# Kernel optimization log

Measured on AMD Instinct MI355X. Metric: run time of the kernel, lower is better.

## Reference

```python
import jax, jax.numpy as jnp
import numpy as np

TOPK = 20
BN_EPS = 1e-5
NEG_SLOPE = 0.2  # DGL GAT default leaky_relu slope


def setup_inputs() -> dict:
    B, N, Ft, D = 128, 512, 64, 64
    key = jax.random.key(0)
    ks = jax.random.split(key, 6)
    return {
        "data": jax.random.normal(ks[0], (B, N, Ft), jnp.float32),
        "emb": jax.random.normal(ks[1], (N, D), jnp.float32) * 0.5,
        "fc_w": jax.random.normal(ks[2], (D, Ft), jnp.float32) * (1.0 / np.sqrt(Ft)),
        "fc_b": jnp.zeros((D,), jnp.float32),
        "attn_w": jax.random.normal(ks[3], (4 * D,), jnp.float32) * (1.0 / np.sqrt(4 * D)),
        "attn_b": jnp.zeros((), jnp.float32),
        "bn_gamma": jnp.ones((D,), jnp.float32),
        "bn_beta": jnp.zeros((D,), jnp.float32),
        "out_w": jax.random.normal(ks[4], (D,), jnp.float32) * (1.0 / np.sqrt(D)),
        "out_b": jnp.zeros((), jnp.float32),
    }


def reference(data, emb, fc_w, fc_b, attn_w, attn_b, bn_gamma, bn_beta, out_w, out_b):
    B, N, Ft = data.shape
    D = emb.shape[-1]

    # --- dynamic graph build from detached embeddings (cosine-sim topk) ---
    w = jax.lax.stop_gradient(emb)
    nrm = jnp.linalg.norm(w, axis=-1)
    cos = (w @ w.T) / (nrm[:, None] * nrm[None, :])      # [N, N]
    _, topk_idx = jax.lax.top_k(cos, TOPK)               # [N, TOPK]
    src = topk_idx.reshape(-1)                           # gated_j (message sources)
    dst = jnp.tile(jnp.arange(N), TOPK)                  # gated_i = arange(N).repeat(1,topk).flatten()

    # --- GAT layer: z = W x + b ; edge score from concat([z, emb]) at both ends ---
    z = jnp.einsum("bnf,df->bnd", data, fc_w) + fc_b     # [B, N, D]
    key_feat = jnp.concatenate([z, jnp.broadcast_to(emb, (B, N, D))], axis=-1)  # [B, N, 2D]
    a_src, a_dst = attn_w[: 2 * D], attn_w[2 * D :]
    s_src = jnp.einsum("bnd,d->bn", key_feat, a_src)
    s_dst = jnp.einsum("bnd,d->bn", key_feat, a_dst)
    e = jax.nn.leaky_relu(s_src[:, src] + s_dst[:, dst] + attn_b, NEG_SLOPE)    # [B, E]

    # segment softmax over incoming edges of each dst node (same edges every batch)
    m = jnp.full((B, N), -jnp.inf, e.dtype).at[:, dst].max(e)
    p = jnp.exp(e - m[:, dst])
    denom = jnp.zeros((B, N), e.dtype).at[:, dst].add(p)
    alpha = p / denom[:, dst]                            # [B, E]

    # scatter-aggregate messages
    h = jnp.zeros_like(z).at[:, dst].add(alpha[..., None] * z[:, src])          # [B, N, D]

    # --- trailing dense: mul by embedding, BatchNorm1d over channel D, relu, linear ---
    rst = h * emb[None]                                  # [B, N, D]
    mu = rst.mean(axis=(0, 1))
    var = rst.var(axis=(0, 1))
    rst = jax.nn.relu((rst - mu) / jnp.sqrt(var + BN_EPS) * bn_gamma + bn_beta)
    out = jnp.einsum("bnd,d->bn", rst, out_w) + out_b    # [B, N]
    return out
```

## Files before the change

### kernel.cpp

```cpp
#include <hip/hip_runtime.h>

#define NN 512
#define DD 64
#define TOPK 20
#define BB 128

__global__ __launch_bounds__(256) void k1_pre(const float* __restrict__ data,
                                              const float* __restrict__ emb,
                                              const float* __restrict__ fc_w,
                                              const float* __restrict__ fc_b,
                                              const float* __restrict__ attn_w,
                                              float* __restrict__ es_src,
                                              float* __restrict__ es_dst,
                                              double* __restrict__ gstats,
                                              float* __restrict__ z,
                                              float* __restrict__ zsrc,
                                              float* __restrict__ zdst,
                                              int* __restrict__ topk) {
    __shared__ __align__(16) char smem[34816];
    const int bid = blockIdx.x, t = threadIdx.x;

    if (bid < 512) {
        const int i = bid;
        double* cosrow = (double*)smem;
        double* nrmv   = (double*)(smem + 4096);
        float4* A4     = (float4*)(smem + 8192);
        const float4* e4 = (const float4*)emb;

        if (t < 16) A4[t] = e4[i * 16 + t];
        __syncthreads();

        #pragma unroll
        for (int jj = 0; jj < 2; ++jj) {
            const int j = jj * 256 + t;
            double dot = 0.0, ss = 0.0;
            #pragma unroll
            for (int c = 0; c < 16; ++c) {
                const float4 a = A4[c];
                const float4 b = e4[j * 16 + c];
                dot += (double)a.x * (double)b.x;
                dot += (double)a.y * (double)b.y;
                dot += (double)a.z * (double)b.z;
                dot += (double)a.w * (double)b.w;
                const double vx = b.x, vy = b.y, vz = b.z, vw = b.w;
                ss += vx * vx; ss += vy * vy; ss += vz * vz; ss += vw * vw;
            }
            cosrow[j] = dot;
            nrmv[j]   = sqrt(ss);
        }
        __syncthreads();

        if (t < 64) {
            const int lane = t;
            const double nrm_i = nrmv[i];
            double v[8];
            #pragma unroll
            for (int s = 0; s < 8; ++s)
                v[s] = cosrow[s * 64 + lane] / (nrm_i * nrmv[s * 64 + lane]);

            for (int k = 0; k < TOPK; ++k) {
                double bv = v[0]; int bs = 0;
                #pragma unroll
                for (int s = 1; s < 8; ++s) if (v[s] > bv) { bv = v[s]; bs = s; }
                int bi2 = bs * 64 + lane;
                #pragma unroll
                for (int off = 32; off > 0; off >>= 1) {
                    double ov = __shfl_xor(bv, off);
                    int    oi = __shfl_xor(bi2, off);
                    if (ov > bv || (ov == bv && oi < bi2)) { bv = ov; bi2 = oi; }
                }
                if (lane == 0) topk[i * TOPK + k] = bi2;
                if ((bi2 & 63) == lane) v[bi2 >> 6] = -1e300;
            }
        }
    } else if (bid < 1536) {
        float (*As)[68]  = (float(*)[68])smem;
        float (*WsT)[68] = (float(*)[68])(smem + 17408);
        const long r0 = (long)(bid - 512) * 64;
        const float4* data4 = (const float4*)data;
        const float4* fcw4  = (const float4*)fc_w;

        for (int m = t; m < 1024; m += 256) {
            const int r = m >> 4, c4 = m & 15;
            *(float4*)&As[r][c4 * 4] = data4[(r0 + r) * 16 + c4];
        }
        for (int m = t; m < 1024; m += 256) {
            const int d = m >> 4, f4 = m & 15;
            float4 v = fcw4[d * 16 + f4];
            WsT[f4 * 4 + 0][d] = v.x;
            WsT[f4 * 4 + 1][d] = v.y;
            WsT[f4 * 4 + 2][d] = v.z;
            WsT[f4 * 4 + 3][d] = v.w;
        }
        __syncthreads();

        const int tr = t >> 4, tc = t & 15;
        float acc[4][4] = {};
        for (int k0 = 0; k0 < 64; k0 += 4) {
            float4 a4[4], b4[4];
            #pragma unroll
            for (int i = 0; i < 4; ++i) a4[i] = *(float4*)&As[tr * 4 + i][k0];
            #pragma unroll
            for (int kk = 0; kk < 4; ++kk) b4[kk] = *(float4*)&WsT[k0 + kk][tc * 4];
            #pragma unroll
            for (int i = 0; i < 4; ++i) {
                acc[i][0] += a4[i].x * b4[0].x + a4[i].y * b4[1].x + a4[i].z * b4[2].x + a4[i].w * b4[3].x;
                acc[i][1] += a4[i].x * b4[0].y + a4[i].y * b4[1].y + a4[i].z * b4[2].y + a4[i].w * b4[3].y;
                acc[i][2] += a4[i].x * b4[0].z + a4[i].y * b4[1].z + a4[i].z * b4[2].z + a4[i].w * b4[3].z;
                acc[i][3] += a4[i].x * b4[0].w + a4[i].y * b4[1].w + a4[i].z * b4[2].w + a4[i].w * b4[3].w;
            }
        }
        float bias[4], aw0[4], aw2[4];
        #pragma unroll
        for (int j = 0; j < 4; ++j) {
            bias[j] = fc_b[tc * 4 + j];
            aw0[j]  = attn_w[tc * 4 + j];
            aw2[j]  = attn_w[128 + tc * 4 + j];
        }
        float zb[4][4];
        #pragma unroll
        for (int i = 0; i < 4; ++i) {
            #pragma unroll
            for (int j = 0; j < 4; ++j) zb[i][j] = acc[i][j] + bias[j];
            float4 vv; vv.x = zb[i][0]; vv.y = zb[i][1]; vv.z = zb[i][2]; vv.w = zb[i][3];
            *(float4*)&z[(r0 + tr * 4 + i) * 64 + tc * 4] = vv;
        }
        __syncthreads();

        float (*redA)[17] = (float(*)[17])smem;
        float (*redB)[17] = (float(*)[17])(smem + 4352);
        #pragma unroll
        for (int i = 0; i < 4; ++i) {
            redA[tr * 4 + i][tc] = zb[i][0] * aw0[0] + zb[i][1] * aw0[1] + zb[i][2] * aw0[2] + zb[i][3] * aw0[3];
            redB[tr * 4 + i][tc] = zb[i][0] * aw2[0] + zb[i][1] * aw2[1] + zb[i][2] * aw2[2] + zb[i][3] * aw2[3];
        }
        __syncthreads();
        if (t < 64) {
            float sA = 0.f, sB = 0.f;
            #pragma unroll
            for (int k = 0; k < 16; ++k) { sA += redA[t][k]; sB += redB[t][k]; }
            zsrc[r0 + t] = sA;
            zdst[r0 + t] = sB;
        }
    } else {
        #pragma unroll
        for (int jj = 0; jj < 2; ++jj) {
            const int j = jj * 256 + t;
            float s1 = 0.f, s2 = 0.f;
            #pragma unroll
            for (int c = 0; c < 64; ++c) {
                const float w = emb[j * 64 + c];
                s1 += w * attn_w[64 + c];
                s2 += w * attn_w[192 + c];
            }
            es_src[j] = s1;
            es_dst[j] = s2;
        }
        if (t < 128) gstats[t] = 0.0;
    }
}

__global__ __launch_bounds__(256) void k3_attn(const float* __restrict__ z,
                                               const float* __restrict__ zsrc,
                                               const float* __restrict__ zdst,
                                               const float* __restrict__ es_src,
                                               const float* __restrict__ es_dst,
                                               const int* __restrict__ topk,
                                               const float* __restrict__ emb,
                                               const float* __restrict__ attn_b_p,
                                               float* __restrict__ rst,
                                               double* __restrict__ gstats) {
    __shared__ float  zs[512 * 16];
    __shared__ double alf_pool[2560];
    __shared__ unsigned short sIdx[256 * 20];
    float* alf = (float*)alf_pool;
    const float4* alf4 = (const float4*)alf_pool;

    const int b    = blockIdx.x >> 2;
    const int dq   = blockIdx.x & 3;
    const int doff = dq * 16;
    const int t    = threadIdx.x;
    const float attn_b = *attn_b_p;
    const long b512 = (long)b * NN;

    float4* zs4 = (float4*)zs;
    for (int m = t; m < 2048; m += 256) {
        const int n = m >> 2, c4i = m & 3;
        zs4[m] = *(const float4*)(z + (b512 + n) * 64 + doff + c4i * 4);
    }
    __syncthreads();

    const int c4 = t & 3;
    const int rq = t >> 2;
    double s1[4] = {0,0,0,0}, s2[4] = {0,0,0,0};

    for (int chunk = 0; chunk < 2; ++chunk) {
        {
            const int n = chunk * 256 + t;
            const float sd = zdst[b512 + n] + es_dst[n] + attn_b;
            float ev[TOPK];
            float m0 = -1e30f;
            #pragma unroll
            for (int tt = 0; tt < TOPK; ++tt) {
                const int s = topk[n + tt * NN];
                sIdx[t * TOPK + tt] = (unsigned short)s;
                float e = zsrc[b512 + s] + es_src[s] + sd;
                e = (e >= 0.f) ? e : 0.2f * e;
                ev[tt] = e;
                m0 = fmaxf(m0, e);
            }
            float dsum = 0.f;
            #pragma unroll
            for (int tt = 0; tt < TOPK; ++tt) { ev[tt] = __expf(ev[tt] - m0); dsum += ev[tt]; }
            const float inv = 1.0f / dsum;
            #pragma unroll
            for (int tt = 0; tt < TOPK; ++tt) alf[t * TOPK + tt] = ev[tt] * inv;
        }
        __syncthreads();

        #pragma unroll
        for (int it = 0; it < 4; ++it) {
            const int nl = it * 64 + rq;
            const int n  = chunk * 256 + nl;
            float4 af[5];
            #pragma unroll
            for (int q = 0; q < 5; ++q) af[q] = alf4[nl * 5 + q];
            const float* av = (const float*)af;
            float4 acc = {0.f, 0.f, 0.f, 0.f};
            #pragma unroll
            for (int tt = 0; tt < TOPK; ++tt) {
                const float a = av[tt];
                const float4 zv = zs4[(int)sIdx[nl * TOPK + tt] * 4 + c4];
                acc.x += a * zv.x; acc.y += a * zv.y; acc.z += a * zv.z; acc.w += a * zv.w;
            }
            const float4 ev = *(const float4*)&emb[n * 64 + doff + c4 * 4];
            float4 r;
            r.x = acc.x * ev.x; r.y = acc.y * ev.y; r.z = acc.z * ev.z; r.w = acc.w * ev.w;
            *(float4*)&rst[(b512 + n) * 64 + doff + c4 * 4] = r;
            s1[0] += (double)r.x; s2[0] += (double)r.x * (double)r.x;
            s1[1] += (double)r.y; s2[1] += (double)r.y * (double)r.y;
            s1[2] += (double)r.z; s2[2] += (double)r.z * (double)r.z;
            s1[3] += (double)r.w; s2[3] += (double)r.w * (double)r.w;
        }
        __syncthreads();
    }

    double* r1 = alf_pool;
    double* r2 = alf_pool + 1024;
    #pragma unroll
    for (int j = 0; j < 4; ++j) {
        r1[(c4 * 4 + j) * 64 + rq] = s1[j];
        r2[(c4 * 4 + j) * 64 + rq] = s2[j];
    }
    __syncthreads();
    if (t < 16) {
        double a = 0.0, bb = 0.0;
        for (int q = 0; q < 64; ++q) { a += r1[t * 64 + q]; bb += r2[t * 64 + q]; }
        atomicAdd(&gstats[doff + t], a);
        atomicAdd(&gstats[64 + doff + t], bb);
    }
}

__global__ __launch_bounds__(256) void k5_out(const float* __restrict__ rst,
                                              const double* __restrict__ gstats,
                                              const float* __restrict__ gamma,
                                              const float* __restrict__ beta,
                                              const float* __restrict__ out_w,
                                              const float* __restrict__ out_b_p,
                                              float* __restrict__ out) {
    __shared__ float scv[64], biv[64];
    const int t = threadIdx.x;
    if (t < 64) {
        const double M = (double)BB * (double)NN;
        const double s  = gstats[t];
        const double s2 = gstats[64 + t];
        const double mu  = s / M;
        const double var = s2 / M - mu * mu;
        const float scale = (float)((double)gamma[t] / sqrt(var + 1e-5));
        scv[t] = scale;
        biv[t] = beta[t] - (float)mu * scale;
    }
    __syncthreads();

    const int wid = t >> 6, lane = t & 63;
    const float sc = scv[lane], bi = biv[lane], ow = out_w[lane];
    const float ob = *out_b_p;
    const long rowbase = (long)blockIdx.x * 16 + wid * 4;
    float v[4];
    #pragma unroll
    for (int rr = 0; rr < 4; ++rr)
        v[rr] = fmaxf(rst[(rowbase + rr) * 64 + lane] * sc + bi, 0.f) * ow;
    #pragma unroll
    for (int off = 32; off > 0; off >>= 1)
        #pragma unroll
        for (int rr = 0; rr < 4; ++rr) v[rr] += __shfl_down(v[rr], off);
    if (lane == 0)
        #pragma unroll
        for (int rr = 0; rr < 4; ++rr) out[rowbase + rr] = v[rr] + ob;
}

extern "C" void kernel_launch(void* const* d_in, const int* in_sizes, int n_in,
                              void* d_out, int out_size, void* d_ws, size_t ws_size,
                              hipStream_t stream) {
    const float* data   = (const float*)d_in[0];
    const float* emb    = (const float*)d_in[1];
    const float* fc_w   = (const float*)d_in[2];
    const float* fc_b   = (const float*)d_in[3];
    const float* attn_w = (const float*)d_in[4];
    const float* attn_b = (const float*)d_in[5];
    const float* gamma  = (const float*)d_in[6];
    const float* beta   = (const float*)d_in[7];
    const float* out_w  = (const float*)d_in[8];
    const float* out_b  = (const float*)d_in[9];
    float* out = (float*)d_out;

    char* ws = (char*)d_ws;
    float*  z      = (float*) (ws + 0);
    float*  rst    = (float*) (ws + 16777216);
    float*  zsrc   = (float*) (ws + 33554432);
    float*  zdst   = (float*) (ws + 33816576);
    int*    topk   = (int*)   (ws + 34078720);
    float*  es_src = (float*) (ws + 34119680);
    float*  es_dst = (float*) (ws + 34121728);
    double* gstats = (double*)(ws + 34123776);

    k1_pre<<<1537, 256, 0, stream>>>(data, emb, fc_w, fc_b, attn_w,
                                     es_src, es_dst, gstats,
                                     z, zsrc, zdst, topk);
    k3_attn<<<BB * 4, 256, 0, stream>>>(z, zsrc, zdst, es_src, es_dst, topk, emb,
                                        attn_b, rst, gstats);
    k5_out<<<4096, 256, 0, stream>>>(rst, gstats, gamma, beta, out_w, out_b, out);
}
```

Baseline: 136.7 us.

## Have each thread own one node's full 16-channel slice in attention aggregation

The attention kernel now gives each thread one destination node and all 16 channels of the block's quarter. It keeps the softmax weights and neighbor indices in registers instead of staging alpha and index arrays through shared memory. The z tile is stored in LDS with a padded stride of 17 floats to reduce bank conflicts on the gathered rows, and two of the per-chunk barriers are removed. The cost is much higher register pressure: 32 double accumulators plus 16 float accumulators per thread. The rst stores also become per-thread strided writes, and the final BatchNorm statistics reduction is serialized over 256 entries per channel.

```diff
diff --git a/kernel.cpp b/kernel.cpp
--- a/kernel.cpp
+++ b/kernel.cpp
@@ -170,11 +170,9 @@
                                                const float* __restrict__ attn_b_p,
                                                float* __restrict__ rst,
                                                double* __restrict__ gstats) {
-    __shared__ float  zs[512 * 16];
-    __shared__ double alf_pool[2560];
-    __shared__ unsigned short sIdx[256 * 20];
-    float* alf = (float*)alf_pool;
-    const float4* alf4 = (const float4*)alf_pool;
+    __shared__ __align__(16) char smem[34816];
+    float*  zs = (float*)smem;
+    double* rr = (double*)smem;
 
     const int b    = blockIdx.x >> 2;
     const int dq   = blockIdx.x & 3;
@@ -183,81 +181,86 @@
     const float attn_b = *attn_b_p;
     const long b512 = (long)b * NN;
 
-    float4* zs4 = (float4*)zs;
     for (int m = t; m < 2048; m += 256) {
         const int n = m >> 2, c4i = m & 3;
-        zs4[m] = *(const float4*)(z + (b512 + n) * 64 + doff + c4i * 4);
-    }
-    __syncthreads();
-
-    const int c4 = t & 3;
-    const int rq = t >> 2;
-    double s1[4] = {0,0,0,0}, s2[4] = {0,0,0,0};
-
+        const float4 v = *(const float4*)(z + (b512 + n) * 64 + doff + c4i * 4);
+        float* p = &zs[n * 17 + c4i * 4];
+        p[0] = v.x; p[1] = v.y; p[2] = v.z; p[3] = v.w;
+    }
+
+    double s1[16], s2[16];
+    #pragma unroll
+    for (int d = 0; d < 16; ++d) { s1[d] = 0.0; s2[d] = 0.0; }
+
+    bool synced = false;
+    #pragma unroll
     for (int chunk = 0; chunk < 2; ++chunk) {
-        {
-            const int n = chunk * 256 + t;
-            const float sd = zdst[b512 + n] + es_dst[n] + attn_b;
-            float ev[TOPK];
-            float m0 = -1e30f;
-            #pragma unroll
-            for (int tt = 0; tt < TOPK; ++tt) {
-                const int s = topk[n + tt * NN];
-                sIdx[t * TOPK + tt] = (unsigned short)s;
-                float e = zsrc[b512 + s] + es_src[s] + sd;
-                e = (e >= 0.f) ? e : 0.2f * e;
-                ev[tt] = e;
-                m0 = fmaxf(m0, e);
-            }
-            float dsum = 0.f;
-            #pragma unroll
-            for (int tt = 0; tt < TOPK; ++tt) { ev[tt] = __expf(ev[tt] - m0); dsum += ev[tt]; }
-            const float inv = 1.0f / dsum;
-            #pragma unroll
-            for (int tt = 0; tt < TOPK; ++tt) alf[t * TOPK + tt] = ev[tt] * inv;
-        }
-        __syncthreads();
-
-        #pragma unroll
-        for (int it = 0; it < 4; ++it) {
-            const int nl = it * 64 + rq;
-            const int n  = chunk * 256 + nl;
-            float4 af[5];
-            #pragma unroll
-            for (int q = 0; q < 5; ++q) af[q] = alf4[nl * 5 + q];
-            const float* av = (const float*)af;
-            float4 acc = {0.f, 0.f, 0.f, 0.f};
-            #pragma unroll
-            for (int tt = 0; tt < TOPK; ++tt) {
-                const float a = av[tt];
-                const float4 zv = zs4[(int)sIdx[nl * TOPK + tt] * 4 + c4];
-                acc.x += a * zv.x; acc.y += a * zv.y; acc.z += a * zv.z; acc.w += a * zv.w;
-            }
-            const float4 ev = *(const float4*)&emb[n * 64 + doff + c4 * 4];
-            float4 r;
-            r.x = acc.x * ev.x; r.y = acc.y * ev.y; r.z = acc.z * ev.z; r.w = acc.w * ev.w;
-            *(float4*)&rst[(b512 + n) * 64 + doff + c4 * 4] = r;
-            s1[0] += (double)r.x; s2[0] += (double)r.x * (double)r.x;
-            s1[1] += (double)r.y; s2[1] += (double)r.y * (double)r.y;
-            s1[2] += (double)r.z; s2[2] += (double)r.z * (double)r.z;
-            s1[3] += (double)r.w; s2[3] += (double)r.w * (double)r.w;
-        }
-        __syncthreads();
-    }
-
-    double* r1 = alf_pool;
-    double* r2 = alf_pool + 1024;
-    #pragma unroll
-    for (int j = 0; j < 4; ++j) {
-        r1[(c4 * 4 + j) * 64 + rq] = s1[j];
-        r2[(c4 * 4 + j) * 64 + rq] = s2[j];
-    }
+        const int n = chunk * 256 + t;
+
+        const float sd = zdst[b512 + n] + es_dst[n] + attn_b;
+        int   idxr[TOPK];
+        float ev[TOPK];
+        float m0 = -1e30f;
+        #pragma unroll
+        for (int tt = 0; tt < TOPK; ++tt) {
+            const int s = topk[n + tt * NN];
+            idxr[tt] = s;
+            float e = zsrc[b512 + s] + es_src[s] + sd;
+            e = (e >= 0.f) ? e : 0.2f * e;
+            ev[tt] = e;
+            m0 = fmaxf(m0, e);
+        }
+        float dsum = 0.f;
+        #pragma unroll
+        for (int tt = 0; tt < TOPK; ++tt) { ev[tt] = __expf(ev[tt] - m0); dsum += ev[tt]; }
+        const float inv = 1.0f / dsum;
+
+        if (!synced) { __syncthreads(); synced = true; }
+
+        float acc[16];
+        #pragma unroll
+        for (int d = 0; d < 16; ++d) acc[d] = 0.f;
+        #pragma unroll
+        for (int tt = 0; tt < TOPK; ++tt) {
+            const float a = ev[tt] * inv;
+            const float* row = &zs[idxr[tt] * 17];
+            #pragma unroll
+            for (int d = 0; d < 16; ++d) acc[d] += a * row[d];
+        }
+
+        const float* eb = &emb[n * 64 + doff];
+        float r[16];
+        #pragma unroll
+        for (int d = 0; d < 16; ++d) {
+            r[d] = acc[d] * eb[d];
+            s1[d] += (double)r[d];
+            s2[d] += (double)r[d] * (double)r[d];
+        }
+        float* ro = &rst[(b512 + n) * 64 + doff];
+        #pragma unroll
+        for (int q = 0; q < 4; ++q) {
+            float4 vv; vv.x = r[q*4+0]; vv.y = r[q*4+1]; vv.z = r[q*4+2]; vv.w = r[q*4+3];
+            *(float4*)&ro[q * 4] = vv;
+        }
+    }
+
+    __syncthreads();
+    #pragma unroll
+    for (int d = 0; d < 16; ++d) rr[d * 256 + t] = s1[d];
     __syncthreads();
     if (t < 16) {
-        double a = 0.0, bb = 0.0;
-        for (int q = 0; q < 64; ++q) { a += r1[t * 64 + q]; bb += r2[t * 64 + q]; }
+        double a = 0.0;
+        for (int q = 0; q < 256; ++q) a += rr[t * 256 + q];
         atomicAdd(&gstats[doff + t], a);
-        atomicAdd(&gstats[64 + doff + t], bb);
+    }
+    __syncthreads();
+    #pragma unroll
+    for (int d = 0; d < 16; ++d) rr[d * 256 + t] = s2[d];
+    __syncthreads();
+    if (t < 16) {
+        double a = 0.0;
+        for (int q = 0; q < 256; ++q) a += rr[t * 256 + q];
+        atomicAdd(&gstats[64 + doff + t], a);
     }
 }
 
```

Result: slower. 144.7 us (+5.8%).
